# Performance work log

Hardware: AMD Instinct MI355X
Metric: run time of the kernel (lower is better)

Reference implementation:

```python
import jax, jax.numpy as jnp
import numpy as np

NUM_HEADS = 16
HEAD_DIM = 64
D_DEC = 1024
D_ENC = 1024
R = 256  # kv_lora_rank
LN_EPS = 1e-5


def setup_inputs() -> dict:
    key = jax.random.key(0)
    ks = jax.random.split(key, 8)
    B, SQ, SK = 4, 2048, 4096
    query = jax.random.normal(ks[0], (B, SQ, D_DEC), dtype=jnp.float32)
    encoder_output = jax.random.normal(ks[1], (B, SK, D_ENC), dtype=jnp.float32)
    s = 0.02
    Wq = jax.random.normal(ks[2], (NUM_HEADS * HEAD_DIM, D_DEC), dtype=jnp.float32) * s
    Wkva = jax.random.normal(ks[3], (R, D_ENC), dtype=jnp.float32) * s
    ln_g = jnp.ones((R,), dtype=jnp.float32)
    ln_b = jnp.zeros((R,), dtype=jnp.float32)
    Wkvb = jax.random.normal(ks[4], (NUM_HEADS * 2 * HEAD_DIM, R), dtype=jnp.float32) * s
    Wout = jax.random.normal(ks[5], (D_DEC, NUM_HEADS * HEAD_DIM), dtype=jnp.float32) * s
    return {"query": query, "encoder_output": encoder_output, "Wq": Wq,
            "Wkva": Wkva, "ln_g": ln_g, "ln_b": ln_b, "Wkvb": Wkvb, "Wout": Wout}


def reference(query, encoder_output, Wq, Wkva, ln_g, ln_b, Wkvb, Wout):
    B, SQ, _ = query.shape
    SK = encoder_output.shape[1]
    H, Dh = NUM_HEADS, HEAD_DIM

    # q projection -> [B, H, SQ, Dh]
    q = jnp.einsum('bsd,ed->bse', query, Wq).reshape(B, SQ, H, Dh).transpose(0, 2, 1, 3)

    # low-rank KV compression + layernorm
    c = jnp.einsum('bsd,rd->bsr', encoder_output, Wkva)  # [B, SK, R]
    mu = jnp.mean(c, axis=-1, keepdims=True)
    var = jnp.mean(jnp.square(c - mu), axis=-1, keepdims=True)
    c = (c - mu) * jax.lax.rsqrt(var + LN_EPS) * ln_g + ln_b

    # decompress to K,V: [B, SK, H, 2*Dh] -> split
    kv = jnp.einsum('bsr,er->bse', c, Wkvb).reshape(B, SK, H, 2 * Dh).transpose(0, 2, 1, 3)
    k, v = kv[..., :Dh], kv[..., Dh:]

    scale = 1.0 / np.sqrt(Dh).astype(np.float32)
    scores = jnp.einsum('bhqd,bhkd->bhqk', q, k) * scale
    attn = jax.nn.softmax(scores, axis=-1)  # dropout is identity in eval / p=0
    o = jnp.einsum('bhqk,bhkd->bhqd', attn, v)
    o = o.transpose(0, 2, 1, 3).reshape(B, SQ, H * Dh)
    return jnp.einsum('bse,de->bsd', o, Wout)
```

## Files before the change

kernel.cpp:

```cpp
#include <hip/hip_runtime.h>

#define LOG2E 1.4426950408889634f

typedef __attribute__((ext_vector_type(8))) short short8;
typedef __attribute__((ext_vector_type(4))) float f32x4;
typedef __attribute__((ext_vector_type(16))) float f32x16;
typedef __attribute__((ext_vector_type(4))) unsigned u32x4;

__device__ inline unsigned short f2bf(float f) {
  unsigned u = __float_as_uint(f);
  u += 0x7fffu + ((u >> 16) & 1u);
  return (unsigned short)(u >> 16);
}

#define MFMA16(a, b, c) __builtin_amdgcn_mfma_f32_16x16x32_bf16((a), (b), (c), 0, 0, 0)
#define MFMA32(a, b, c) __builtin_amdgcn_mfma_f32_32x32x16_bf16((a), (b), (c), 0, 0, 0)

#define GLDS16(gp, lp)                                                              \
  __builtin_amdgcn_global_load_lds((const __attribute__((address_space(1))) void*)(gp), \
                                   (__attribute__((address_space(3))) void*)(lp), 16, 0, 0)

__device__ inline f32x4 zero4() {
  f32x4 z = {0.f, 0.f, 0.f, 0.f};
  return z;
}
__device__ inline f32x16 zero16() {
  f32x16 z = {0.f, 0.f, 0.f, 0.f, 0.f, 0.f, 0.f, 0.f, 0.f, 0.f, 0.f, 0.f, 0.f, 0.f, 0.f, 0.f};
  return z;
}
__device__ inline unsigned cvtpk_bf16(float a, float b) {
  unsigned r;
  asm("v_cvt_pk_bf16_f32 %0, %1, %2" : "=v"(r) : "v"(a), "v"(b));
  return r;
}
__device__ inline void plswap(unsigned& a, unsigned& b) {
  asm("v_permlane32_swap_b32 %0, %1" : "+v"(a), "+v"(b));
}

__global__ __launch_bounds__(256) void k_cast4(
    const float* __restrict__ wq, const float* __restrict__ wo,
    const float* __restrict__ wb, const float* __restrict__ wa,
    unsigned short* __restrict__ wqo, unsigned short* __restrict__ woo,
    unsigned short* __restrict__ wbo, unsigned short* __restrict__ wao) {
  int i = (blockIdx.x * 256 + threadIdx.x) * 4;
  const float* src;
  unsigned short* dst;
  int off;
  if (i < 1048576) { src = wq; dst = wqo; off = i; }
  else if (i < 2097152) { src = wo; dst = woo; off = i - 1048576; }
  else if (i < 2621440) { src = wb; dst = wbo; off = i - 2097152; }
  else { src = wa; dst = wao; off = i - 2621440; }
  float4 v = *(const float4*)(src + off);
  unsigned lo = (unsigned)f2bf(v.x) | ((unsigned)f2bf(v.y) << 16);
  unsigned hi = (unsigned)f2bf(v.z) | ((unsigned)f2bf(v.w) << 16);
  *(uint2*)(dst + off) = make_uint2(lo, hi);
}

__global__ __launch_bounds__(256, 2) void k_qproj(const float* __restrict__ A,
                                                  const unsigned short* __restrict__ Bw,
                                                  unsigned short* __restrict__ Qout) {
  __shared__ __align__(16) short As[128 * 32];
  __shared__ __align__(16) short Bs[128 * 32];
  const int K = 1024;
  int tid = threadIdx.x;
  int w = tid >> 6, lane = tid & 63, quad = lane >> 4, c = lane & 15;
  int m0 = blockIdx.x * 128, n0 = blockIdx.y * 128;
  int wm = (w >> 1) * 64, wn = (w & 1) * 64;
  int rsub = lane >> 2, csub = (lane & 3) * 8;
  f32x4 acc[4][4];
#pragma unroll
  for (int i = 0; i < 4; i++)
#pragma unroll
    for (int j = 0; j < 4; j++) acc[i][j] = zero4();

  for (int k0 = 0; k0 < K; k0 += 32) {
#pragma unroll
    for (int i = 0; i < 2; i++) {
      int seg = w * 2 + i;
      const float* Ap = A + (size_t)(m0 + seg * 16 + rsub) * K + k0 + csub;
      float4 va = *(const float4*)Ap;
      float4 vb2 = *(const float4*)(Ap + 4);
      u32x4 pk = {cvtpk_bf16(va.x, va.y), cvtpk_bf16(va.z, va.w),
                  cvtpk_bf16(vb2.x, vb2.y), cvtpk_bf16(vb2.z, vb2.w)};
      *(u32x4*)((char*)As + seg * 1024 + lane * 16) = pk;
    }
#pragma unroll
    for (int i = 0; i < 2; i++) {
      int seg = w * 2 + i;
      int bo = seg * 1024 + lane * 16;
      int row = bo >> 6, col = (bo & 63) >> 1;
      GLDS16(Bw + (size_t)(n0 + row) * K + k0 + col, (char*)Bs + seg * 1024);
    }
    __syncthreads();
    short8 af[4], bfr[4];
#pragma unroll
    for (int i = 0; i < 4; i++) {
      af[i] = *(const short8*)&As[(wm + i * 16 + c) * 32 + quad * 8];
      bfr[i] = *(const short8*)&Bs[(wn + i * 16 + c) * 32 + quad * 8];
    }
#pragma unroll
    for (int mi = 0; mi < 4; mi++)
#pragma unroll
      for (int ni = 0; ni < 4; ni++) acc[mi][ni] = MFMA16(af[mi], bfr[ni], acc[mi][ni]);
    __syncthreads();
  }
  const float scale = 0.125f * LOG2E;
#pragma unroll
  for (int mi = 0; mi < 4; mi++) {
    int rowb = m0 + wm + mi * 16 + quad * 4;
#pragma unroll
    for (int ni = 0; ni < 4; ni++) {
      int col = n0 + wn + ni * 16 + c;
      int h = col >> 6, d = col & 63;
#pragma unroll
      for (int r = 0; r < 4; r++) {
        int row = rowb + r;
        int b = row >> 11, sq = row & 2047;
        Qout[(((size_t)(b * 16 + h)) * 2048 + sq) * 64 + d] = f2bf(acc[mi][ni][r] * scale);
      }
    }
  }
}

__global__ __launch_bounds__(256, 2) void k_cln(const float* __restrict__ E,
                                                const unsigned short* __restrict__ Wa,
                                                const float* __restrict__ g, const float* __restrict__ bb,
                                                unsigned short* __restrict__ Cout) {
  __shared__ __align__(16) short As[64 * 32];
  __shared__ __align__(16) short Bs[256 * 32];
  __shared__ float redS[4][64], redQ[4][64];
  __shared__ float gS[256], bS[256];
  const int K = 1024;
  int tid = threadIdx.x;
  int w = tid >> 6, lane = tid & 63, quad = lane >> 4, c = lane & 15;
  int m0 = blockIdx.x * 64;
  int rsub = lane >> 2, csub = (lane & 3) * 8;
  gS[tid] = g[tid];
  bS[tid] = bb[tid];
  f32x4 acc[4][4];
#pragma unroll
  for (int i = 0; i < 4; i++)
#pragma unroll
    for (int j = 0; j < 4; j++) acc[i][j] = zero4();

  for (int k0 = 0; k0 < K; k0 += 32) {
    {
      const float* Ep = E + (size_t)(m0 + w * 16 + rsub) * K + k0 + csub;
      float4 va = *(const float4*)Ep;
      float4 vb2 = *(const float4*)(Ep + 4);
      u32x4 pk = {cvtpk_bf16(va.x, va.y), cvtpk_bf16(va.z, va.w),
                  cvtpk_bf16(vb2.x, vb2.y), cvtpk_bf16(vb2.z, vb2.w)};
      *(u32x4*)((char*)As + w * 1024 + lane * 16) = pk;
    }
#pragma unroll
    for (int i = 0; i < 4; i++) {
      int seg = w * 4 + i;
      int bo = seg * 1024 + lane * 16;
      int row = bo >> 6, col = (bo & 63) >> 1;
      GLDS16(Wa + (size_t)row * K + k0 + col, (char*)Bs + seg * 1024);
    }
    __syncthreads();
    short8 af[4], bfr[4];
#pragma unroll
    for (int i = 0; i < 4; i++) {
      af[i] = *(const short8*)&As[(i * 16 + c) * 32 + quad * 8];
      bfr[i] = *(const short8*)&Bs[(w * 64 + i * 16 + c) * 32 + quad * 8];
    }
#pragma unroll
    for (int mi = 0; mi < 4; mi++)
#pragma unroll
      for (int ni = 0; ni < 4; ni++) acc[mi][ni] = MFMA16(af[mi], bfr[ni], acc[mi][ni]);
    __syncthreads();
  }
  float ps[4][4], pq[4][4];
#pragma unroll
  for (int mi = 0; mi < 4; mi++)
#pragma unroll
    for (int r = 0; r < 4; r++) {
      float s = 0.f, q = 0.f;
#pragma unroll
      for (int ni = 0; ni < 4; ni++) {
        float x = acc[mi][ni][r];
        s += x;
        q += x * x;
      }
      for (int m = 1; m < 16; m <<= 1) {
        s += __shfl_xor(s, m, 64);
        q += __shfl_xor(q, m, 64);
      }
      ps[mi][r] = s;
      pq[mi][r] = q;
    }
  if (c == 0) {
#pragma unroll
    for (int mi = 0; mi < 4; mi++)
#pragma unroll
      for (int r = 0; r < 4; r++) {
        int row = mi * 16 + quad * 4 + r;
        redS[w][row] = ps[mi][r];
        redQ[w][row] = pq[mi][r];
      }
  }
  __syncthreads();
  float muv[4][4], rsv[4][4];
#pragma unroll
  for (int mi = 0; mi < 4; mi++)
#pragma unroll
    for (int r = 0; r < 4; r++) {
      int row = mi * 16 + quad * 4 + r;
      float S = redS[0][row] + redS[1][row] + redS[2][row] + redS[3][row];
      float Q = redQ[0][row] + redQ[1][row] + redQ[2][row] + redQ[3][row];
      float mu = S * (1.f / 256.f);
      float var = Q * (1.f / 256.f) - mu * mu;
      muv[mi][r] = mu;
      rsv[mi][r] = rsqrtf(var + 1e-5f);
    }
#pragma unroll
  for (int mi = 0; mi < 4; mi++)
#pragma unroll
    for (int ni = 0; ni < 4; ni++) {
      int col = w * 64 + ni * 16 + c;
#pragma unroll
      for (int r = 0; r < 4; r++) {
        int row = m0 + mi * 16 + quad * 4 + r;
        float y = (acc[mi][ni][r] - muv[mi][r]) * rsv[mi][r] * gS[col] + bS[col];
        Cout[(size_t)row * 256 + col] = f2bf(y);
      }
    }
}

__global__ __launch_bounds__(256, 2) void k_kv(const unsigned short* __restrict__ A,
                                               const unsigned short* __restrict__ Bw,
                                               unsigned short* __restrict__ Kb,
                                               unsigned short* __restrict__ Vb) {
  __shared__ __align__(16) short As[128 * 32];
  __shared__ __align__(16) short Bs[128 * 32];
  const int K = 256;
  int tid = threadIdx.x;
  int w = tid >> 6, lane = tid & 63, quad = lane >> 4, c = lane & 15;
  int m0 = blockIdx.x * 128, n0 = blockIdx.y * 128;
  int wm = (w >> 1) * 64, wn = (w & 1) * 64;
  f32x4 acc[4][4];
#pragma unroll
  for (int i = 0; i < 4; i++)
#pragma unroll
    for (int j = 0; j < 4; j++) acc[i][j] = zero4();

  for (int k0 = 0; k0 < K; k0 += 32) {
#pragma unroll
    for (int i = 0; i < 2; i++) {
      int seg = w * 2 + i;
      int bo = seg * 1024 + lane * 16;
      int row = bo >> 6, col = (bo & 63) >> 1;
      GLDS16(A + (size_t)(m0 + row) * K + k0 + col, (char*)As + seg * 1024);
      GLDS16(Bw + (size_t)(n0 + row) * K + k0 + col, (char*)Bs + seg * 1024);
    }
    __syncthreads();
    short8 af[4], bfr[4];
#pragma unroll
    for (int i = 0; i < 4; i++) {
      af[i] = *(const short8*)&As[(wm + i * 16 + c) * 32 + quad * 8];
      bfr[i] = *(const short8*)&Bs[(wn + i * 16 + c) * 32 + quad * 8];
    }
#pragma unroll
    for (int mi = 0; mi < 4; mi++)
#pragma unroll
      for (int ni = 0; ni < 4; ni++) acc[mi][ni] = MFMA16(af[mi], bfr[ni], acc[mi][ni]);
    __syncthreads();
  }
#pragma unroll
  for (int mi = 0; mi < 4; mi++) {
    int rowb = m0 + wm + mi * 16 + quad * 4;
    int b = rowb >> 12;
    int sk0 = rowb & 4095;
    int kt = sk0 >> 6, ki0 = sk0 & 63;
    int sg = ((wm + mi * 16) & 63) >> 4;
    int khi = quad >> 1;
    int j0 = (quad & 1) * 4;
#pragma unroll
    for (int ni = 0; ni < 4; ni++) {
      int col = n0 + wn + ni * 16 + c;
      int h = col >> 7, rr = col & 127;
      size_t base = ((size_t)(b * 16 + h)) * 262144 + (size_t)kt * 4096;
      if (rr < 64) {
        int d = rr;
        int ds = d >> 4, dhi = (d >> 3) & 1, j = d & 7;
#pragma unroll
        for (int r = 0; r < 4; r++) {
          int ki = ki0 + r;
          int half = ki >> 5, l31k = ki & 31;
          Kb[base + (size_t)((half * 4 + ds) * 64 + l31k + 32 * dhi) * 8 + j] = f2bf(acc[mi][ni][r]);
        }
      } else {
        int d = rr - 64;
        int dt = d >> 5;
        unsigned lo = (unsigned)f2bf(acc[mi][ni][0]) | ((unsigned)f2bf(acc[mi][ni][1]) << 16);
        unsigned hi = (unsigned)f2bf(acc[mi][ni][2]) | ((unsigned)f2bf(acc[mi][ni][3]) << 16);
        *(uint2*)(Vb + base + (size_t)((dt * 4 + sg) * 64 + (d & 31) + 32 * khi) * 8 + j0) =
            make_uint2(lo, hi);
      }
    }
  }
}

__device__ __forceinline__ void attn_tile(const char* Kl, const char* Vl,
                                          const short8 (&qf)[4], f32x16 (&O)[2], float& lp) {
#pragma unroll
  for (int h = 0; h < 2; h++) {
    short8 kf[4];
#pragma unroll
    for (int ds = 0; ds < 4; ds++) kf[ds] = *(const short8*)(Kl + (h * 4 + ds) * 1024);
    f32x16 S = zero16();
    __builtin_amdgcn_s_setprio(1);
#pragma unroll
    for (int ds = 0; ds < 4; ds++) S = MFMA32(kf[ds], qf[ds], S);
    __builtin_amdgcn_s_setprio(0);
    float lpa = 0.f, lpb = 0.f;
    unsigned u[8];
#pragma unroll
    for (int m = 0; m < 8; m++) {
      float p0 = __builtin_amdgcn_exp2f(S[2 * m]);
      float p1 = __builtin_amdgcn_exp2f(S[2 * m + 1]);
      if (m & 1) lpb += p0 + p1; else lpa += p0 + p1;
      u[m] = cvtpk_bf16(p0, p1);
    }
    lp += lpa + lpb;
    plswap(u[0], u[2]);
    plswap(u[1], u[3]);
    plswap(u[4], u[6]);
    plswap(u[5], u[7]);
    u32x4 w0 = {u[0], u[1], u[2], u[3]};
    u32x4 w1 = {u[4], u[5], u[6], u[7]};
    short8 paf0 = __builtin_bit_cast(short8, w0);
    short8 paf1 = __builtin_bit_cast(short8, w1);
    __builtin_amdgcn_s_setprio(1);
#pragma unroll
    for (int dt = 0; dt < 2; dt++) {
      short8 vf0 = *(const short8*)(Vl + (dt * 4 + h * 2 + 0) * 1024);
      short8 vf1 = *(const short8*)(Vl + (dt * 4 + h * 2 + 1) * 1024);
      O[dt] = MFMA32(paf0, vf0, O[dt]);
      O[dt] = MFMA32(paf1, vf1, O[dt]);
    }
    __builtin_amdgcn_s_setprio(0);
  }
}

__global__ __launch_bounds__(256, 4) void k_attn(const unsigned short* __restrict__ Qb,
                                                 const unsigned short* __restrict__ Kb,
                                                 const unsigned short* __restrict__ Vb,
                                                 unsigned short* __restrict__ Ob) {
  __shared__ __align__(16) short KA[8192];
  __shared__ __align__(16) short KB[8192];
  int tid = threadIdx.x;
  int w = tid >> 6, lane = tid & 63;
  int l31 = lane & 31, hi = lane >> 5;
  int qt = blockIdx.x, bh = blockIdx.y;

  const char* Kg = (const char*)Kb + (size_t)bh * 524288;
  const char* Vg = (const char*)Vb + (size_t)bh * 524288;
  int ldsseg = (w < 2) ? w * 4 : 8 + (w - 2) * 4;
  const char* sgbase = ((w < 2) ? Kg + (w * 4) * 1024 : Vg + ((w - 2) * 4) * 1024) + lane * 16;

  const unsigned short* Qrow = Qb + ((size_t)bh * 2048 + qt * 128 + w * 32 + l31) * 64 + hi * 8;
  short8 qf[4];
#pragma unroll
  for (int ds = 0; ds < 4; ds++) qf[ds] = *(const short8*)(Qrow + ds * 16);

  f32x16 O[2];
  float lp = 0.f;
#pragma unroll
  for (int j = 0; j < 2; j++) O[j] = zero16();

#pragma unroll
  for (int i = 0; i < 4; i++) GLDS16(sgbase + i * 1024, (char*)KA + (ldsseg + i) * 1024);
  sgbase += 8192;
  __syncthreads();

  for (int kt2 = 0; kt2 < 64; kt2 += 2) {
    {
#pragma unroll
      for (int i = 0; i < 4; i++)
        GLDS16(sgbase + i * 1024, (char*)KB + (ldsseg + i) * 1024);
      sgbase += 8192;
      attn_tile((const char*)KA + lane * 16, (const char*)KA + lane * 16 + 8192, qf, O, lp);
      __syncthreads();
    }
    {
      if (kt2 < 62) {
#pragma unroll
        for (int i = 0; i < 4; i++)
          GLDS16(sgbase + i * 1024, (char*)KA + (ldsseg + i) * 1024);
        sgbase += 8192;
      }
      attn_tile((const char*)KB + lane * 16, (const char*)KB + lane * 16 + 8192, qf, O, lp);
      __syncthreads();
    }
  }

  lp += __shfl_xor(lp, 32, 64);
  int b = bh >> 4, hh = bh & 15;
#pragma unroll
  for (int r = 0; r < 16; r++) {
    int qrow = (r & 3) + 8 * (r >> 2) + 4 * hi;
    float inv = __builtin_amdgcn_rcpf(__shfl(lp, qrow, 64));
    size_t orow = ((size_t)b * 2048 + qt * 128 + w * 32 + qrow) * 1024 + hh * 64 + l31;
    Ob[orow] = f2bf(O[0][r] * inv);
    Ob[orow + 32] = f2bf(O[1][r] * inv);
  }
}

__global__ __launch_bounds__(256, 2) void k_out(const unsigned short* __restrict__ A,
                                                const unsigned short* __restrict__ Bw,
                                                float* __restrict__ Out) {
  __shared__ __align__(16) short As[128 * 32];
  __shared__ __align__(16) short Bs[128 * 32];
  const int K = 1024;
  int tid = threadIdx.x;
  int w = tid >> 6, lane = tid & 63, quad = lane >> 4, c = lane & 15;
  int m0 = blockIdx.x * 128, n0 = blockIdx.y * 128;
  int wm = (w >> 1) * 64, wn = (w & 1) * 64;
  f32x4 acc[4][4];
#pragma unroll
  for (int i = 0; i < 4; i++)
#pragma unroll
    for (int j = 0; j < 4; j++) acc[i][j] = zero4();

  for (int k0 = 0; k0 < K; k0 += 32) {
#pragma unroll
    for (int i = 0; i < 2; i++) {
      int seg = w * 2 + i;
      int bo = seg * 1024 + lane * 16;
      int row = bo >> 6, col = (bo & 63) >> 1;
      GLDS16(A + (size_t)(m0 + row) * K + k0 + col, (char*)As + seg * 1024);
      GLDS16(Bw + (size_t)(n0 + row) * K + k0 + col, (char*)Bs + seg * 1024);
    }
    __syncthreads();
    short8 af[4], bfr[4];
#pragma unroll
    for (int i = 0; i < 4; i++) {
      af[i] = *(const short8*)&As[(wm + i * 16 + c) * 32 + quad * 8];
      bfr[i] = *(const short8*)&Bs[(wn + i * 16 + c) * 32 + quad * 8];
    }
#pragma unroll
    for (int mi = 0; mi < 4; mi++)
#pragma unroll
      for (int ni = 0; ni < 4; ni++) acc[mi][ni] = MFMA16(af[mi], bfr[ni], acc[mi][ni]);
    __syncthreads();
  }
#pragma unroll
  for (int mi = 0; mi < 4; mi++) {
    int rowb = m0 + wm + mi * 16 + quad * 4;
#pragma unroll
    for (int ni = 0; ni < 4; ni++) {
      int col = n0 + wn + ni * 16 + c;
#pragma unroll
      for (int r = 0; r < 4; r++) Out[(size_t)(rowb + r) * 1024 + col] = acc[mi][ni][r];
    }
  }
}

extern "C" void kernel_launch(void* const* d_in, const int* in_sizes, int n_in,
                              void* d_out, int out_size, void* d_ws, size_t ws_size,
                              hipStream_t stream) {
  const float* query = (const float*)d_in[0];
  const float* enc = (const float*)d_in[1];
  const float* Wq = (const float*)d_in[2];
  const float* Wkva = (const float*)d_in[3];
  const float* ln_g = (const float*)d_in[4];
  const float* ln_b = (const float*)d_in[5];
  const float* Wkvb = (const float*)d_in[6];
  const float* Wout = (const float*)d_in[7];
  if (ws_size < 81264640) return;

  char* ws = (char*)d_ws;
  unsigned short* wq_bf = (unsigned short*)(ws + 0);
  unsigned short* wa_bf = (unsigned short*)(ws + 2097152);
  unsigned short* wb_bf = (unsigned short*)(ws + 2621440);
  unsigned short* wo_bf = (unsigned short*)(ws + 3670016);
  unsigned short* qproj = (unsigned short*)(ws + 5767168);
  unsigned short* cln = (unsigned short*)(ws + 22544384);
  unsigned short* vbuf = (unsigned short*)(ws + 30932992);
  unsigned short* obuf = (unsigned short*)(ws + 64487424);
  unsigned short* kbuf = (unsigned short*)d_out;

  k_cast4<<<2816, 256, 0, stream>>>(Wq, Wout, Wkvb, Wkva, wq_bf, wo_bf, wb_bf, wa_bf);

  k_qproj<<<dim3(64, 8), 256, 0, stream>>>(query, wq_bf, qproj);
  k_cln<<<256, 256, 0, stream>>>(enc, wa_bf, ln_g, ln_b, cln);
  k_kv<<<dim3(128, 16), 256, 0, stream>>>(cln, wb_bf, kbuf, vbuf);
  k_attn<<<dim3(16, 64), 256, 0, stream>>>(qproj, kbuf, vbuf, obuf);
  k_out<<<dim3(64, 8), 256, 0, stream>>>(obuf, wo_bf, (float*)d_out);
}
```

Before: 455.9 us.

## Pre-cast query to bf16 and load Q-proj A tiles via direct LDS DMA

The fp32 query is now converted to bf16 in the weight-cast kernel and stored in a workspace buffer that is later reused for the attention output. The Q projection then loads its A tiles with global_load_lds straight into LDS instead of loading fp32 and converting in registers. The attention inner loop also drops its s_setprio priority bumps around the MFMA groups. This adds an extra full pass that reads the query in fp32 and writes it in bf16, in exchange for halving the GEMM's A-tile reads and taking the conversion out of the GEMM's critical path.

```diff
diff --git a/kernel.cpp b/kernel.cpp
--- a/kernel.cpp
+++ b/kernel.cpp
@@ -37,26 +37,27 @@
   asm("v_permlane32_swap_b32 %0, %1" : "+v"(a), "+v"(b));
 }
 
-__global__ __launch_bounds__(256) void k_cast4(
-    const float* __restrict__ wq, const float* __restrict__ wo,
+__global__ __launch_bounds__(256) void k_cast5(
+    const float* __restrict__ q, const float* __restrict__ wq, const float* __restrict__ wo,
     const float* __restrict__ wb, const float* __restrict__ wa,
-    unsigned short* __restrict__ wqo, unsigned short* __restrict__ woo,
+    unsigned short* __restrict__ qo, unsigned short* __restrict__ wqo, unsigned short* __restrict__ woo,
     unsigned short* __restrict__ wbo, unsigned short* __restrict__ wao) {
   int i = (blockIdx.x * 256 + threadIdx.x) * 4;
   const float* src;
   unsigned short* dst;
   int off;
-  if (i < 1048576) { src = wq; dst = wqo; off = i; }
-  else if (i < 2097152) { src = wo; dst = woo; off = i - 1048576; }
-  else if (i < 2621440) { src = wb; dst = wbo; off = i - 2097152; }
-  else { src = wa; dst = wao; off = i - 2621440; }
+  if (i < 8388608) { src = q; dst = qo; off = i; }
+  else if (i < 9437184) { src = wq; dst = wqo; off = i - 8388608; }
+  else if (i < 10485760) { src = wo; dst = woo; off = i - 9437184; }
+  else if (i < 11010048) { src = wb; dst = wbo; off = i - 10485760; }
+  else { src = wa; dst = wao; off = i - 11010048; }
   float4 v = *(const float4*)(src + off);
   unsigned lo = (unsigned)f2bf(v.x) | ((unsigned)f2bf(v.y) << 16);
   unsigned hi = (unsigned)f2bf(v.z) | ((unsigned)f2bf(v.w) << 16);
   *(uint2*)(dst + off) = make_uint2(lo, hi);
 }
 
-__global__ __launch_bounds__(256, 2) void k_qproj(const float* __restrict__ A,
+__global__ __launch_bounds__(256, 2) void k_qproj(const unsigned short* __restrict__ A,
                                                   const unsigned short* __restrict__ Bw,
                                                   unsigned short* __restrict__ Qout) {
   __shared__ __align__(16) short As[128 * 32];
@@ -66,7 +67,6 @@
   int w = tid >> 6, lane = tid & 63, quad = lane >> 4, c = lane & 15;
   int m0 = blockIdx.x * 128, n0 = blockIdx.y * 128;
   int wm = (w >> 1) * 64, wn = (w & 1) * 64;
-  int rsub = lane >> 2, csub = (lane & 3) * 8;
   f32x4 acc[4][4];
 #pragma unroll
   for (int i = 0; i < 4; i++)
@@ -74,21 +74,12 @@
     for (int j = 0; j < 4; j++) acc[i][j] = zero4();
 
   for (int k0 = 0; k0 < K; k0 += 32) {
-#pragma unroll
-    for (int i = 0; i < 2; i++) {
-      int seg = w * 2 + i;
-      const float* Ap = A + (size_t)(m0 + seg * 16 + rsub) * K + k0 + csub;
-      float4 va = *(const float4*)Ap;
-      float4 vb2 = *(const float4*)(Ap + 4);
-      u32x4 pk = {cvtpk_bf16(va.x, va.y), cvtpk_bf16(va.z, va.w),
-                  cvtpk_bf16(vb2.x, vb2.y), cvtpk_bf16(vb2.z, vb2.w)};
-      *(u32x4*)((char*)As + seg * 1024 + lane * 16) = pk;
-    }
 #pragma unroll
     for (int i = 0; i < 2; i++) {
       int seg = w * 2 + i;
       int bo = seg * 1024 + lane * 16;
       int row = bo >> 6, col = (bo & 63) >> 1;
+      GLDS16(A + (size_t)(m0 + row) * K + k0 + col, (char*)As + seg * 1024);
       GLDS16(Bw + (size_t)(n0 + row) * K + k0 + col, (char*)Bs + seg * 1024);
     }
     __syncthreads();
@@ -311,10 +302,8 @@
 #pragma unroll
     for (int ds = 0; ds < 4; ds++) kf[ds] = *(const short8*)(Kl + (h * 4 + ds) * 1024);
     f32x16 S = zero16();
-    __builtin_amdgcn_s_setprio(1);
 #pragma unroll
     for (int ds = 0; ds < 4; ds++) S = MFMA32(kf[ds], qf[ds], S);
-    __builtin_amdgcn_s_setprio(0);
     float lpa = 0.f, lpb = 0.f;
     unsigned u[8];
 #pragma unroll
@@ -333,7 +322,6 @@
     u32x4 w1 = {u[4], u[5], u[6], u[7]};
     short8 paf0 = __builtin_bit_cast(short8, w0);
     short8 paf1 = __builtin_bit_cast(short8, w1);
-    __builtin_amdgcn_s_setprio(1);
 #pragma unroll
     for (int dt = 0; dt < 2; dt++) {
       short8 vf0 = *(const short8*)(Vl + (dt * 4 + h * 2 + 0) * 1024);
@@ -341,7 +329,6 @@
       O[dt] = MFMA32(paf0, vf0, O[dt]);
       O[dt] = MFMA32(paf1, vf1, O[dt]);
     }
-    __builtin_amdgcn_s_setprio(0);
   }
 }
 
@@ -480,14 +467,15 @@
   unsigned short* qproj = (unsigned short*)(ws + 5767168);
   unsigned short* cln = (unsigned short*)(ws + 22544384);
   unsigned short* vbuf = (unsigned short*)(ws + 30932992);
-  unsigned short* obuf = (unsigned short*)(ws + 64487424);
+  unsigned short* qin_o = (unsigned short*)(ws + 64487424);
   unsigned short* kbuf = (unsigned short*)d_out;
 
-  k_cast4<<<2816, 256, 0, stream>>>(Wq, Wout, Wkvb, Wkva, wq_bf, wo_bf, wb_bf, wa_bf);
-
-  k_qproj<<<dim3(64, 8), 256, 0, stream>>>(query, wq_bf, qproj);
+  k_cast5<<<11008, 256, 0, stream>>>(query, Wq, Wout, Wkvb, Wkva,
+                                     qin_o, wq_bf, wo_bf, wb_bf, wa_bf);
+
+  k_qproj<<<dim3(64, 8), 256, 0, stream>>>(qin_o, wq_bf, qproj);
   k_cln<<<256, 256, 0, stream>>>(enc, wa_bf, ln_g, ln_b, cln);
   k_kv<<<dim3(128, 16), 256, 0, stream>>>(cln, wb_bf, kbuf, vbuf);
-  k_attn<<<dim3(16, 64), 256, 0, stream>>>(qproj, kbuf, vbuf, obuf);
-  k_out<<<dim3(64, 8), 256, 0, stream>>>(obuf, wo_bf, (float*)d_out);
-}
+  k_attn<<<dim3(16, 64), 256, 0, stream>>>(qproj, kbuf, vbuf, qin_o);
+  k_out<<<dim3(64, 8), 256, 0, stream>>>(qin_o, wo_bf, (float*)d_out);
+}
```

Result: faster. 405.9 us (-11.0%).
